# Kernel tuning notes

Measured on AMD Instinct MI355X. Metric: run time of the kernel, lower is better.

The kernel has to match this reference:

```python
import jax, jax.numpy as jnp
import numpy as np
from jax import lax

B, T, E, H = 4096, 200, 64, 64
N_USER, N_ITEM = 100000, 100000
ATT_H1, ATT_H2 = 80, 40  # DIN attention MLP sizes
FCN_IN = 4 * E + H  # user + item + hist_sum + item*hist_sum + gru2 final state


def setup_inputs() -> dict:
    key = jax.random.key(0)
    ks = jax.random.split(key, 32)
    s = 0.1
    rn = lambda k, shp: (jax.random.normal(k, shp, dtype=jnp.float32) * s)
    u = jax.random.randint(ks[0], (B,), 0, N_USER)
    i = jax.random.randint(ks[1], (B,), 0, N_ITEM)
    hist_i = jax.random.randint(ks[2], (B, T), 0, N_ITEM)
    sl = jax.random.randint(ks[3], (B,), 1, T + 1)
    mask = (jnp.arange(T)[None, :] < sl[:, None]).astype(jnp.float32)
    inp = dict(u=u, i=i, hist_i=hist_i, mask=mask)
    inp.update(
        item_emb_w=rn(ks[4], (N_ITEM, E)),
        user_emb_w=rn(ks[5], (N_USER, E)),
        # GRU1 (input dim E, hidden H): gates [r,z] fused, candidate separate (TF GRUCell layout)
        gru1_Wg=rn(ks[6], (E, 2 * H)), gru1_Ug=rn(ks[7], (H, 2 * H)), gru1_bg=jnp.zeros((2 * H,), jnp.float32),
        gru1_Wc=rn(ks[8], (E, H)), gru1_Uc=rn(ks[9], (H, H)), gru1_bc=jnp.zeros((H,), jnp.float32),
        # DIN attention MLP over [q, k, q-k, q*k]
        Wa1=rn(ks[10], (4 * H, ATT_H1)), ba1=jnp.zeros((ATT_H1,), jnp.float32),
        Wa2=rn(ks[11], (ATT_H1, ATT_H2)), ba2=jnp.zeros((ATT_H2,), jnp.float32),
        Wa3=rn(ks[12], (ATT_H2, 1)), ba3=jnp.zeros((1,), jnp.float32),
        # GRU2 (input dim H, hidden H)
        gru2_Wg=rn(ks[13], (H, 2 * H)), gru2_Ug=rn(ks[14], (H, 2 * H)), gru2_bg=jnp.zeros((2 * H,), jnp.float32),
        gru2_Wc=rn(ks[15], (H, H)), gru2_Uc=rn(ks[16], (H, H)), gru2_bc=jnp.zeros((H,), jnp.float32),
        # fcn_net: dense(2E) -> prelu -> dense(40) -> prelu -> dense(1)
        W1=rn(ks[17], (FCN_IN, 2 * E)), b1=jnp.zeros((2 * E,), jnp.float32), p1=jnp.full((2 * E,), 0.25, jnp.float32),
        W2=rn(ks[18], (2 * E, 40)), b2=jnp.zeros((40,), jnp.float32), p2=jnp.full((40,), 0.25, jnp.float32),
        W3=rn(ks[19], (40, 1)), b3=jnp.zeros((1,), jnp.float32),
    )
    return inp


def _gru(x, mask, Wg, Ug, bg, Wc, Uc, bc):
    """TF GRUCell semantics; mask freezes state past sequence length. x: [B,T,D]."""
    xg = jnp.einsum('btd,dh->bth', x, Wg) + bg  # precompute input projections
    xc = jnp.einsum('btd,dh->bth', x, Wc) + bc
    h0 = jnp.zeros((x.shape[0], Uc.shape[0]), dtype=x.dtype)

    def step(h, inp):
        xg_t, xc_t, m = inp
        r, z = jnp.split(jax.nn.sigmoid(xg_t + h @ Ug), 2, axis=-1)
        c = jnp.tanh(xc_t + (r * h) @ Uc)
        h_new = z * h + (1.0 - z) * c
        h = m[:, None] * h_new + (1.0 - m[:, None]) * h
        return h, h

    hT, hs = lax.scan(step, h0, (xg.transpose(1, 0, 2), xc.transpose(1, 0, 2), mask.T))
    return jnp.transpose(hs, (1, 0, 2)), hT  # [B,T,H], [B,H]


def _prelu(x, a):
    return jnp.where(x >= 0, x, a * x)


def reference(u, i, hist_i, mask, item_emb_w, user_emb_w,
              gru1_Wg, gru1_Ug, gru1_bg, gru1_Wc, gru1_Uc, gru1_bc,
              Wa1, ba1, Wa2, ba2, Wa3, ba3,
              gru2_Wg, gru2_Ug, gru2_bg, gru2_Wc, gru2_Uc, gru2_bc,
              W1, b1, p1, W2, b2, p2, W3, b3):
    item_eb = item_emb_w[i]            # [B,E]
    user_eb = user_emb_w[u]            # [B,E]
    hist_eb = item_emb_w[hist_i]       # [B,T,E]
    hist_sum = jnp.sum(hist_eb, axis=1)  # original uses unmasked reduce_sum

    # GRU encoder over history
    rnn1, _ = _gru(hist_eb, mask, gru1_Wg, gru1_Ug, gru1_bg, gru1_Wc, gru1_Uc, gru1_bc)

    # DIN-style attention: target item queries GRU1 states
    q = jnp.broadcast_to(item_eb[:, None, :], rnn1.shape)  # [B,T,H] (E==H)
    din = jnp.concatenate([q, rnn1, q - rnn1, q * rnn1], axis=-1)  # [B,T,4H]
    d1 = jax.nn.sigmoid(din @ Wa1 + ba1)
    d2 = jax.nn.sigmoid(d1 @ Wa2 + ba2)
    scores = (d2 @ Wa3 + ba3)[..., 0]  # [B,T]
    scores = jnp.where(mask > 0, scores, -1e9)
    alpha = jax.nn.softmax(scores, axis=-1)  # [B,T]

    # second GRU over attention-weighted states
    att_in = rnn1 * alpha[..., None]
    _, final2 = _gru(att_in, mask, gru2_Wg, gru2_Ug, gru2_bg, gru2_Wc, gru2_Uc, gru2_bc)

    # fcn_net on concatenated features
    inp = jnp.concatenate([user_eb, item_eb, hist_sum, item_eb * hist_sum, final2], axis=-1)
    h1 = _prelu(inp @ W1 + b1, p1)
    h2 = _prelu(h1 @ W2 + b2, p2)
    logits = (h2 @ W3 + b3)[:, 0]  # [B]
    return logits
```

## Files before the change

kernel.cpp:

```cpp
#include <hip/hip_runtime.h>

#define BB 4096
#define TT 200

typedef unsigned short u16;
typedef unsigned int   u32;
typedef unsigned short u16x8 __attribute__((ext_vector_type(8)));
typedef short s16x8 __attribute__((ext_vector_type(8)));
typedef float f32x4 __attribute__((ext_vector_type(4)));

__device__ __forceinline__ float bf2f(u16 u){ union{unsigned u; float f;} v; v.u=((unsigned)u)<<16; return v.f; }
__device__ __forceinline__ u16 f2bf(float f){ union{float f; unsigned u;} v; v.f=f; unsigned r=v.u + 0x7FFFu + ((v.u>>16)&1u); return (u16)(r>>16); }
__device__ __forceinline__ float sigm(float x){ return 1.0f/(1.0f+__expf(-x)); }
__device__ __forceinline__ float tanh_(float x){ return 1.0f - 2.0f/(1.0f+__expf(2.0f*x)); }

#define MFMA16(a,b,c) __builtin_amdgcn_mfma_f32_16x16x32_bf16((a),(b),(c),0,0,0)

__device__ __forceinline__ void split8(const f32x4 a, const f32x4 b, s16x8 &hi, s16x8 &lo){
#pragma unroll
  for (int j=0;j<4;j++){
    float v=a[j]; u16 h=(u16)(__float_as_uint(v)>>16);
    hi[j]=(short)h; lo[j]=(short)f2bf(v-bf2f(h));
    v=b[j]; h=(u16)(__float_as_uint(v)>>16);
    hi[j+4]=(short)h; lo[j+4]=(short)f2bf(v-bf2f(h));
  }
}


__global__ void hist_sum_kernel(const int* __restrict__ hist, const float* __restrict__ emb,
                                float* __restrict__ hs){
  int tid = blockIdx.x*256 + threadIdx.x;
  int b = tid>>3, cg = (tid&7)*8;
  float acc[8];
#pragma unroll
  for (int j=0;j<8;j++) acc[j]=0.0f;
  for (int t=0;t<TT;t++){
    int idx = hist[(size_t)b*TT+t];
    f32x4 v0=*(const f32x4*)(emb+(size_t)idx*64+cg);
    f32x4 v1=*(const f32x4*)(emb+(size_t)idx*64+cg+4);
#pragma unroll
    for (int j=0;j<4;j++){ acc[j]+=v0[j]; acc[j+4]+=v1[j]; }
  }
#pragma unroll
  for (int j=0;j<8;j++) hs[(size_t)b*64+cg+j]=acc[j];
}

__global__ __launch_bounds__(256,1) void scan1_kernel(
    const int* __restrict__ hist, const float* __restrict__ mask, const float* __restrict__ emb,
    const float* __restrict__ Wg, const float* __restrict__ Ug, const float* __restrict__ bg,
    const float* __restrict__ Wc, const float* __restrict__ Uc, const float* __restrict__ bc,
    int* __restrict__ len_g, u16* __restrict__ rnn1)
{
  __shared__ float h1buf[16][68];
  __shared__ float pbuf [16][68];
  __shared__ int   lenL [16];
  const int tid=threadIdx.x;
  const int w=tid>>6, lane=tid&63, q=lane>>4, mm=lane&15;
  const int g=blockIdx.x, b0=g*16, pb_m=b0+mm;

  if (w==0){
    int cnt=0;
    for (int t=q*50;t<q*50+50;t++) cnt += (mask[(size_t)pb_m*TT+t]!=0.0f);
    cnt += __shfl_xor(cnt,16);
    cnt += __shfl_xor(cnt,32);
    if (lane<16){ lenL[lane]=cnt; len_g[b0+lane]=cnt; }
  }
  for (int ii=tid; ii<16*68; ii+=256) (&h1buf[0][0])[ii]=0.0f;
  __syncthreads();

  int lenq[4];
#pragma unroll
  for (int r=0;r<4;r++) lenq[r]=lenL[q*4+r];
  int maxlen=1;
  for (int i=0;i<16;i++) maxlen=(lenL[i]>maxlen)?lenL[i]:maxlen;

  const int nr=16*w+mm, nz=64+16*w+mm;
  s16x8 wgr[4], wgz[4], wcf[4];
#pragma unroll
  for (int c=0;c<4;c++){
    s16x8 fr,fz,fc;
#pragma unroll
    for (int j=0;j<8;j++){
      int k=32*c+q*8+j;
      fr[j]=(short)f2bf((k<64)?Wg[(size_t)k*128+nr]:Ug[(size_t)(k-64)*128+nr]);
      fz[j]=(short)f2bf((k<64)?Wg[(size_t)k*128+nz]:Ug[(size_t)(k-64)*128+nz]);
      fc[j]=(short)f2bf((k<64)?Wc[(size_t)k*64+nr]:Uc[(size_t)(k-64)*64+nr]);
    }
    wgr[c]=fr; wgz[c]=fz; wcf[c]=fc;
  }
  const float bgr=bg[nr], bgz=bg[nz], bcv=bc[nr];

  auto load_x=[&](int t, s16x8 &a0, s16x8 &a1){
    int idx = hist[(size_t)pb_m*TT+t];
    const float* p=emb+(size_t)idx*64;
    f32x4 v0=*(const f32x4*)(p+q*8),    v1=*(const f32x4*)(p+q*8+4);
    f32x4 v2=*(const f32x4*)(p+32+q*8), v3=*(const f32x4*)(p+32+q*8+4);
    s16x8 t0,t1;
#pragma unroll
    for (int j=0;j<4;j++){
      t0[j]=(short)f2bf(v0[j]); t0[j+4]=(short)f2bf(v1[j]);
      t1[j]=(short)f2bf(v2[j]); t1[j+4]=(short)f2bf(v3[j]);
    }
    a0=t0; a1=t1;
  };

  s16x8 xf0,xf1;
  load_x(0,xf0,xf1);
  for (int t=0;t<maxlen;t++){
    s16x8 nx0,nx1;
    { int tn=(t+1<maxlen)?(t+1):(maxlen-1); load_x(tn,nx0,nx1); }

    f32x4 hA0=*(const f32x4*)&h1buf[mm][q*8];
    f32x4 hA1=*(const f32x4*)&h1buf[mm][q*8+4];
    f32x4 hB0=*(const f32x4*)&h1buf[mm][32+q*8];
    f32x4 hB1=*(const f32x4*)&h1buf[mm][32+q*8+4];
    s16x8 hhi0,hlo0,hhi1,hlo1;
    split8(hA0,hA1,hhi0,hlo0);
    split8(hB0,hB1,hhi1,hlo1);

    f32x4 ar={0.0f,0.0f,0.0f,0.0f}, az={0.0f,0.0f,0.0f,0.0f};
    ar=MFMA16(xf0 ,wgr[0],ar); az=MFMA16(xf0 ,wgz[0],az);
    ar=MFMA16(xf1 ,wgr[1],ar); az=MFMA16(xf1 ,wgz[1],az);
    ar=MFMA16(hhi0,wgr[2],ar); az=MFMA16(hhi0,wgz[2],az);
    ar=MFMA16(hhi1,wgr[3],ar); az=MFMA16(hhi1,wgz[3],az);
    ar=MFMA16(hlo0,wgr[2],ar); az=MFMA16(hlo0,wgz[2],az);
    ar=MFMA16(hlo1,wgr[3],ar); az=MFMA16(hlo1,wgz[3],az);

    float zs[4], hv[4];
#pragma unroll
    for (int r=0;r<4;r++){
      float rg=sigm(ar[r]+bgr);
      float hp=h1buf[q*4+r][16*w+mm];
      hv[r]=hp;
      pbuf[q*4+r][16*w+mm]=rg*hp;
      zs[r]=sigm(az[r]+bgz);
    }
    __syncthreads();

    f32x4 pA0=*(const f32x4*)&pbuf[mm][q*8];
    f32x4 pA1=*(const f32x4*)&pbuf[mm][q*8+4];
    f32x4 pB0=*(const f32x4*)&pbuf[mm][32+q*8];
    f32x4 pB1=*(const f32x4*)&pbuf[mm][32+q*8+4];
    s16x8 phi0,plo0,phi1,plo1;
    split8(pA0,pA1,phi0,plo0);
    split8(pB0,pB1,phi1,plo1);

    f32x4 ac={0.0f,0.0f,0.0f,0.0f};
    ac=MFMA16(xf0 ,wcf[0],ac);
    ac=MFMA16(xf1 ,wcf[1],ac);
    ac=MFMA16(phi0,wcf[2],ac);
    ac=MFMA16(phi1,wcf[3],ac);
    ac=MFMA16(plo0,wcf[2],ac);
    ac=MFMA16(plo1,wcf[3],ac);
#pragma unroll
    for (int r=0;r<4;r++){
      float c=tanh_(ac[r]+bcv);
      float z=zs[r];
      float hn=z*hv[r]+(1.0f-z)*c;
      if (t>=lenq[r]) hn=hv[r];
      h1buf[q*4+r][16*w+mm]=hn;
      rnn1[((size_t)(b0+q*4+r)*TT+t)*64 + 16*w+mm]=f2bf(hn);
    }
    __syncthreads();
    xf0=nx0; xf1=nx1;
  }
}

__global__ __launch_bounds__(64,1) void attn_kernel(
    const int* __restrict__ iidx, const float* __restrict__ emb, const u16* __restrict__ rnn1,
    const float* __restrict__ Wa1, const float* __restrict__ ba1,
    const float* __restrict__ Wa2, const float* __restrict__ ba2,
    const float* __restrict__ Wa3, const float* __restrict__ ba3,
    const int* __restrict__ len_g, float* __restrict__ scores)
{
  __shared__ u16 d1buf[16][104];
  const int lane=threadIdx.x, q=lane>>4, mm=lane&15;
  const int b=blockIdx.x;
  const int L=len_g[b];

  s16x8 w1k[5][2], wd[5][2];
#pragma unroll
  for (int nt=0;nt<5;nt++)
#pragma unroll
    for (int c=0;c<2;c++){
      s16x8 f1,f2;
#pragma unroll
      for (int j=0;j<8;j++){
        int k=32*c+q*8+j, n=16*nt+mm;
        f1[j]=(short)f2bf(Wa1[(size_t)(64+k)*80+n] - Wa1[(size_t)(128+k)*80+n]);
        f2[j]=(short)f2bf(Wa1[(size_t)(192+k)*80+n]);
      }
      w1k[nt][c]=f1; wd[nt][c]=f2;
    }
  s16x8 w2f[3][3];
#pragma unroll
  for (int nt=0;nt<3;nt++)
#pragma unroll
    for (int c=0;c<3;c++){
      s16x8 f;
#pragma unroll
      for (int j=0;j<8;j++){
        int k=32*c+q*8+j, n=16*nt+mm;
        f[j]=(short)((k<80 && n<40)?f2bf(Wa2[(size_t)k*40+n]):0);
      }
      w2f[nt][c]=f;
    }
  float ba2v[3], w3v[3];
#pragma unroll
  for (int nt=0;nt<3;nt++){ int n=16*nt+mm; ba2v[nt]=(n<40)?ba2[n]:0.0f; w3v[nt]=(n<40)?Wa3[n]:0.0f; }
  const float ba3v=ba3[0];

  const int ib=iidx[b];
  float qv0[8], qv1[8];
  s16x8 aq0,aq1;
#pragma unroll
  for (int j=0;j<8;j++){
    qv0[j]=emb[(size_t)ib*64+q*8+j];
    qv1[j]=emb[(size_t)ib*64+32+q*8+j];
    aq0[j]=(short)f2bf(qv0[j]); aq1[j]=(short)f2bf(qv1[j]);
  }
  float pre[5];
#pragma unroll
  for (int nt=0;nt<5;nt++){
    int n=16*nt+mm;
    s16x8 bp0,bp1;
#pragma unroll
    for (int j=0;j<8;j++){
      int k=q*8+j, k2=32+q*8+j;
      bp0[j]=(short)f2bf(Wa1[(size_t)k *80+n]+Wa1[(size_t)(128+k )*80+n]);
      bp1[j]=(short)f2bf(Wa1[(size_t)k2*80+n]+Wa1[(size_t)(128+k2)*80+n]);
    }
    f32x4 a={0.0f,0.0f,0.0f,0.0f};
    a=MFMA16(aq0,bp0,a); a=MFMA16(aq1,bp1,a);
    pre[nt]=a[0]+ba1[n];
  }

  for (int ii=lane; ii<16*104; ii+=64) (&d1buf[0][0])[ii]=0;
  __syncthreads();

  const int nch=(L+15)>>4;
  for (int ch=0; ch<nch; ch++){
    int t0=ch*16;
    size_t base=((size_t)b*TT + t0+mm)*64;
    s16x8 kf0=*(const s16x8*)(rnn1+base+q*8);
    s16x8 kf1=*(const s16x8*)(rnn1+base+32+q*8);
    s16x8 kq0,kq1;
#pragma unroll
    for (int j=0;j<8;j++){
      kq0[j]=(short)f2bf(bf2f((u16)kf0[j])*qv0[j]);
      kq1[j]=(short)f2bf(bf2f((u16)kf1[j])*qv1[j]);
    }
    f32x4 acc[5];
#pragma unroll
    for (int nt=0;nt<5;nt++){
      f32x4 a={pre[nt],pre[nt],pre[nt],pre[nt]};
      a=MFMA16(kf0,w1k[nt][0],a); a=MFMA16(kf1,w1k[nt][1],a);
      a=MFMA16(kq0,wd[nt][0],a);  a=MFMA16(kq1,wd[nt][1],a);
      acc[nt]=a;
    }
#pragma unroll
    for (int nt=0;nt<5;nt++)
#pragma unroll
      for (int r=0;r<4;r++)
        d1buf[q*4+r][16*nt+mm]=f2bf(sigm(acc[nt][r]));
    __syncthreads();
    s16x8 a0=*(const s16x8*)&d1buf[mm][q*8];
    s16x8 a1=*(const s16x8*)&d1buf[mm][32+q*8];
    s16x8 a2=*(const s16x8*)&d1buf[mm][64+q*8];
    f32x4 acc2[3];
#pragma unroll
    for (int nt=0;nt<3;nt++){
      f32x4 a={0.0f,0.0f,0.0f,0.0f};
      a=MFMA16(a0,w2f[nt][0],a); a=MFMA16(a1,w2f[nt][1],a); a=MFMA16(a2,w2f[nt][2],a);
      acc2[nt]=a;
    }
    float part[4];
#pragma unroll
    for (int r=0;r<4;r++){
      float s=0.0f;
#pragma unroll
      for (int nt=0;nt<3;nt++) s+=sigm(acc2[nt][r]+ba2v[nt])*w3v[nt];
      part[r]=s;
    }
#pragma unroll
    for (int d=1;d<16;d<<=1)
#pragma unroll
      for (int r=0;r<4;r++) part[r]+=__shfl_xor(part[r],d);
    if (mm==0){
#pragma unroll
      for (int r=0;r<4;r++){ int t=t0+q*4+r; if (t<TT) scores[(size_t)b*TT+t]=part[r]+ba3v; }
    }
    __syncthreads();
  }
}

__global__ __launch_bounds__(64,1) void softmax_kernel(const int* __restrict__ len_g, float* __restrict__ sc){
  const int b=blockIdx.x, lane=threadIdx.x;
  const int L=len_g[b];
  float mx=-3e38f;
  for (int t=lane;t<L;t+=64) mx=fmaxf(mx,sc[(size_t)b*TT+t]);
#pragma unroll
  for (int d=1;d<64;d<<=1) mx=fmaxf(mx,__shfl_xor(mx,d));
  float sm=0.0f;
  for (int t=lane;t<L;t+=64) sm+=__expf(sc[(size_t)b*TT+t]-mx);
#pragma unroll
  for (int d=1;d<64;d<<=1) sm+=__shfl_xor(sm,d);
  float inv=1.0f/sm;
  for (int t=lane;t<TT;t+=64){
    float v=(t<L)?__expf(sc[(size_t)b*TT+t]-mx)*inv:0.0f;
    sc[(size_t)b*TT+t]=v;
  }
}

__global__ __launch_bounds__(256,1) void scan2_kernel(
    const u16* __restrict__ rnn1, const float* __restrict__ alpha, const int* __restrict__ len_g,
    const float* __restrict__ Wg, const float* __restrict__ Ug, const float* __restrict__ bg,
    const float* __restrict__ Wc, const float* __restrict__ Uc, const float* __restrict__ bc,
    float* __restrict__ f2)
{
  __shared__ float h2buf[16][68];
  __shared__ float pbuf [16][68];
  __shared__ int   lenL [16];
  const int tid=threadIdx.x;
  const int w=tid>>6, lane=tid&63, q=lane>>4, mm=lane&15;
  const int g=blockIdx.x, b0=g*16, pb_m=b0+mm;

  if (tid<16) lenL[tid]=len_g[b0+tid];
  for (int ii=tid; ii<16*68; ii+=256) (&h2buf[0][0])[ii]=0.0f;
  __syncthreads();

  int lenq[4];
#pragma unroll
  for (int r=0;r<4;r++) lenq[r]=lenL[q*4+r];
  int maxlen=1;
  for (int i=0;i<16;i++) maxlen=(lenL[i]>maxlen)?lenL[i]:maxlen;

  const int nr=16*w+mm, nz=64+16*w+mm;
  s16x8 wgr[4], wgz[4], wcf[4];
#pragma unroll
  for (int c=0;c<4;c++){
    s16x8 fr,fz,fc;
#pragma unroll
    for (int j=0;j<8;j++){
      int k=32*c+q*8+j;
      fr[j]=(short)f2bf((k<64)?Wg[(size_t)k*128+nr]:Ug[(size_t)(k-64)*128+nr]);
      fz[j]=(short)f2bf((k<64)?Wg[(size_t)k*128+nz]:Ug[(size_t)(k-64)*128+nz]);
      fc[j]=(short)f2bf((k<64)?Wc[(size_t)k*64+nr]:Uc[(size_t)(k-64)*64+nr]);
    }
    wgr[c]=fr; wgz[c]=fz; wcf[c]=fc;
  }
  const float bgr=bg[nr], bgz=bg[nz], bcv=bc[nr];

  auto load_x=[&](int t, s16x8 &a0, s16x8 &a1){
    size_t base=((size_t)pb_m*TT+t)*64;
    u16x8 k0=*(const u16x8*)(rnn1+base+q*8);
    u16x8 k1=*(const u16x8*)(rnn1+base+32+q*8);
    float al=alpha[(size_t)pb_m*TT+t];
    s16x8 t0,t1;
#pragma unroll
    for (int j=0;j<8;j++){
      t0[j]=(short)f2bf(bf2f(k0[j])*al);
      t1[j]=(short)f2bf(bf2f(k1[j])*al);
    }
    a0=t0; a1=t1;
  };

  s16x8 xf0,xf1;
  load_x(0,xf0,xf1);
  for (int t=0;t<maxlen;t++){
    s16x8 nx0,nx1;
    { int tn=(t+1<maxlen)?(t+1):(maxlen-1); load_x(tn,nx0,nx1); }

    f32x4 hA0=*(const f32x4*)&h2buf[mm][q*8];
    f32x4 hA1=*(const f32x4*)&h2buf[mm][q*8+4];
    f32x4 hB0=*(const f32x4*)&h2buf[mm][32+q*8];
    f32x4 hB1=*(const f32x4*)&h2buf[mm][32+q*8+4];
    s16x8 hhi0,hlo0,hhi1,hlo1;
    split8(hA0,hA1,hhi0,hlo0);
    split8(hB0,hB1,hhi1,hlo1);

    f32x4 ar={0.0f,0.0f,0.0f,0.0f}, az={0.0f,0.0f,0.0f,0.0f};
    ar=MFMA16(xf0 ,wgr[0],ar); az=MFMA16(xf0 ,wgz[0],az);
    ar=MFMA16(xf1 ,wgr[1],ar); az=MFMA16(xf1 ,wgz[1],az);
    ar=MFMA16(hhi0,wgr[2],ar); az=MFMA16(hhi0,wgz[2],az);
    ar=MFMA16(hhi1,wgr[3],ar); az=MFMA16(hhi1,wgz[3],az);
    ar=MFMA16(hlo0,wgr[2],ar); az=MFMA16(hlo0,wgz[2],az);
    ar=MFMA16(hlo1,wgr[3],ar); az=MFMA16(hlo1,wgz[3],az);

    float zs[4], hv[4];
#pragma unroll
    for (int r=0;r<4;r++){
      float rg=sigm(ar[r]+bgr);
      float hp=h2buf[q*4+r][16*w+mm];
      hv[r]=hp;
      pbuf[q*4+r][16*w+mm]=rg*hp;
      zs[r]=sigm(az[r]+bgz);
    }
    __syncthreads();

    f32x4 pA0=*(const f32x4*)&pbuf[mm][q*8];
    f32x4 pA1=*(const f32x4*)&pbuf[mm][q*8+4];
    f32x4 pB0=*(const f32x4*)&pbuf[mm][32+q*8];
    f32x4 pB1=*(const f32x4*)&pbuf[mm][32+q*8+4];
    s16x8 phi0,plo0,phi1,plo1;
    split8(pA0,pA1,phi0,plo0);
    split8(pB0,pB1,phi1,plo1);

    f32x4 ac={0.0f,0.0f,0.0f,0.0f};
    ac=MFMA16(xf0 ,wcf[0],ac);
    ac=MFMA16(xf1 ,wcf[1],ac);
    ac=MFMA16(phi0,wcf[2],ac);
    ac=MFMA16(phi1,wcf[3],ac);
    ac=MFMA16(plo0,wcf[2],ac);
    ac=MFMA16(plo1,wcf[3],ac);
#pragma unroll
    for (int r=0;r<4;r++){
      float c=tanh_(ac[r]+bcv);
      float z=zs[r];
      float hn=z*hv[r]+(1.0f-z)*c;
      if (t>=lenq[r]) hn=hv[r];
      h2buf[q*4+r][16*w+mm]=hn;
    }
    __syncthreads();
    xf0=nx0; xf1=nx1;
  }

#pragma unroll
  for (int r=0;r<4;r++)
    f2[(size_t)(b0+q*4+r)*64 + 16*w+mm]=h2buf[q*4+r][16*w+mm];
}

__global__ __launch_bounds__(64,1) void fcn_kernel(
    const int* __restrict__ uidx, const int* __restrict__ iidx,
    const float* __restrict__ uemb, const float* __restrict__ emb,
    const float* __restrict__ hs, const float* __restrict__ f2,
    const float* __restrict__ Wf1, const float* __restrict__ fb1, const float* __restrict__ fp1,
    const float* __restrict__ Wf2, const float* __restrict__ fb2, const float* __restrict__ fp2,
    const float* __restrict__ Wf3, const float* __restrict__ fb3,
    float* __restrict__ out)
{
  __shared__ float inL[16][320];
  __shared__ u16   h1L[16][128];
  __shared__ float h2o[16][40];
  const int lane=threadIdx.x, q=lane>>4, mm=lane&15;
  const int b0=blockIdx.x*16;

  {
    int row=lane>>2, sub=lane&3;
    int b=b0+row;
    int ub=uidx[b], ibv=iidx[b];
    for (int c=sub*80;c<sub*80+80;c++){
      int seg=c>>6, f=c&63; float v;
      if      (seg==0) v=uemb[(size_t)ub*64+f];
      else if (seg==1) v=emb[(size_t)ibv*64+f];
      else if (seg==2) v=hs[(size_t)b*64+f];
      else if (seg==3) v=emb[(size_t)ibv*64+f]*hs[(size_t)b*64+f];
      else             v=f2[(size_t)b*64+f];
      inL[row][c]=v;
    }
  }
  __syncthreads();

  {
    f32x4 acc1[8];
#pragma unroll
    for (int nt=0;nt<8;nt++) acc1[nt]=f32x4{0.0f,0.0f,0.0f,0.0f};
#pragma unroll
    for (int kc=0;kc<10;kc++){
      s16x8 af;
#pragma unroll
      for (int j=0;j<8;j++) af[j]=(short)f2bf(inL[mm][32*kc+q*8+j]);
#pragma unroll
      for (int nt=0;nt<8;nt++){
        s16x8 bfr;
#pragma unroll
        for (int j=0;j<8;j++) bfr[j]=(short)f2bf(Wf1[(size_t)(32*kc+q*8+j)*128 + 16*nt+mm]);
        acc1[nt]=MFMA16(af,bfr,acc1[nt]);
      }
    }
#pragma unroll
    for (int nt=0;nt<8;nt++)
#pragma unroll
      for (int r=0;r<4;r++){
        int col=16*nt+mm, row=q*4+r;
        float x=acc1[nt][r]+fb1[col];
        float pp=fp1[col];
        h1L[row][col]=f2bf((x>=0.0f)?x:pp*x);
      }
  }
  __syncthreads();

  {
    f32x4 acc2[3];
#pragma unroll
    for (int nt=0;nt<3;nt++) acc2[nt]=f32x4{0.0f,0.0f,0.0f,0.0f};
#pragma unroll
    for (int kc=0;kc<4;kc++){
      s16x8 af=*(const s16x8*)&h1L[mm][32*kc+q*8];
#pragma unroll
      for (int nt=0;nt<3;nt++){
        s16x8 bfr;
#pragma unroll
        for (int j=0;j<8;j++){
          int k=32*kc+q*8+j, n=16*nt+mm;
          bfr[j]=(short)((n<40)?f2bf(Wf2[(size_t)k*40+n]):0);
        }
        acc2[nt]=MFMA16(af,bfr,acc2[nt]);
      }
    }
#pragma unroll
    for (int nt=0;nt<3;nt++)
#pragma unroll
      for (int r=0;r<4;r++){
        int col=16*nt+mm, row=q*4+r;
        if (col<40){
          float x=acc2[nt][r]+fb2[col];
          float pp=fp2[col];
          h2o[row][col]=(x>=0.0f)?x:pp*x;
        }
      }
  }
  __syncthreads();

  {
    int row=lane>>2, sub=lane&3;
    float s=0.0f;
    for (int k=sub;k<40;k+=4) s+=h2o[row][k]*Wf3[k];
    s+=__shfl_xor(s,1); s+=__shfl_xor(s,2);
    if (sub==0) out[b0+row]=s+fb3[0];
  }
}

template<bool F32>
__global__ __launch_bounds__(64,1) void dien_mega_kernel(
    const int* __restrict__ uidx, const int* __restrict__ iidx,
    const int* __restrict__ hist, const void* __restrict__ mask,
    const void* __restrict__ emb,  const void* __restrict__ uemb,
    const void* __restrict__ W1g, const void* __restrict__ U1g, const void* __restrict__ g1bg,
    const void* __restrict__ W1c, const void* __restrict__ U1c, const void* __restrict__ g1bc,
    const void* __restrict__ Wa1, const void* __restrict__ ba1,
    const void* __restrict__ Wa2, const void* __restrict__ ba2,
    const void* __restrict__ Wa3, const void* __restrict__ ba3,
    const void* __restrict__ W2g, const void* __restrict__ U2g, const void* __restrict__ g2bg,
    const void* __restrict__ W2c, const void* __restrict__ U2c, const void* __restrict__ g2bc,
    const void* __restrict__ Wf1, const void* __restrict__ fb1, const void* __restrict__ fp1,
    const void* __restrict__ Wf2, const void* __restrict__ fb2, const void* __restrict__ fp2,
    const void* __restrict__ Wf3, const void* __restrict__ fb3,
    void* __restrict__ outp)
{
  auto LF=[&](const void* p, size_t i)->float {
    return F32 ? ((const float*)p)[i] : bf2f(((const u16*)p)[i]);
  };
  auto LB=[&](const void* p, size_t i)->u16 {
    return F32 ? f2bf(((const float*)p)[i]) : ((const u16*)p)[i];
  };
  auto FR8=[&](const void* p, size_t off)->s16x8 {
    s16x8 f;
    if (F32){
      const float* pp=(const float*)p+off;
      f32x4 a=*(const f32x4*)pp, b=*(const f32x4*)(pp+4);
#pragma unroll
      for (int j=0;j<4;j++){ f[j]=(short)f2bf(a[j]); f[j+4]=(short)f2bf(b[j]); }
    } else {
      f=*(const s16x8*)((const u16*)p+off);
    }
    return f;
  };

  __shared__ float h1buf[16][68];
  __shared__ float h2buf[16][68];
  __shared__ float pbuf [16][68];
  __shared__ u16   d1buf[16][104];
  __shared__ u16   scL  [16][200];
  __shared__ float hsL  [16][64];
  __shared__ s16x8 u2gL [16][64];
  __shared__ s16x8 u2cL [ 8][64];
  __shared__ float h2o  [16][40];
  __shared__ u16   ueL  [16][64];
  __shared__ u16   ieL  [16][64];
  __shared__ int   lenL [16];

  const int lane=threadIdx.x, q=lane>>4, mm=lane&15;
  const int g=blockIdx.x, b0=g*16;
  const int pb_m=b0+mm;

  {
    int cnt=0;
    for (int t=q*50;t<q*50+50;t++) cnt += (LF(mask,(size_t)pb_m*TT+t)!=0.0f);
    cnt += __shfl_xor(cnt,16);
    cnt += __shfl_xor(cnt,32);
    if (lane<16) lenL[lane]=cnt;
  }
  __syncthreads();
  int lenq[4];
#pragma unroll
// ... 401 lines not shown
        a=MFMA16(hlo0,wh0,a);
        a=MFMA16(hlo1,wh1,a);
        ga[nt]=a;
      }
      float zs[4][4], hv[4][4];
#pragma unroll
      for (int nt=0;nt<4;nt++)
#pragma unroll
        for (int r=0;r<4;r++){
          float rg=sigm(ga[nt][r]+b2gv[nt]);
          float h_=h2buf[q*4+r][16*nt+mm];
          hv[nt][r]=h_;
          pbuf[q*4+r][16*nt+mm]=rg*h_;
          zs[nt][r]=sigm(ga[nt+4][r]+b2gv[nt+4]);
        }
      __syncthreads();
      f32x4 pA0=*(const f32x4*)&pbuf[mm][q*8];
      f32x4 pA1=*(const f32x4*)&pbuf[mm][q*8+4];
      f32x4 pB0=*(const f32x4*)&pbuf[mm][32+q*8];
      f32x4 pB1=*(const f32x4*)&pbuf[mm][32+q*8+4];
      s16x8 phi0,plo0,phi1,plo1;
      split8(pA0,pA1,phi0,plo0);
      split8(pB0,pB1,phi1,plo1);
      f32x4 ca[4];
#pragma unroll
      for (int nt=0;nt<4;nt++){
        s16x8 wh0=u2cL[nt*2+0][lane];
        s16x8 wh1=u2cL[nt*2+1][lane];
        f32x4 a={0.0f,0.0f,0.0f,0.0f};
        a=MFMA16(af0 ,wc2x[nt][0],a);
        a=MFMA16(af1 ,wc2x[nt][1],a);
        a=MFMA16(phi0,wh0,a);
        a=MFMA16(phi1,wh1,a);
        a=MFMA16(plo0,wh0,a);
        a=MFMA16(plo1,wh1,a);
        ca[nt]=a;
      }
#pragma unroll
      for (int nt=0;nt<4;nt++)
#pragma unroll
        for (int r=0;r<4;r++){
          float c=tanh_(ca[nt][r]+b2cv[nt]);
          float z=zs[nt][r];
          float hn=z*hv[nt][r]+(1.0f-z)*c;
          if (t>=lenq[r]) hn=hv[nt][r];
          h2buf[q*4+r][16*nt+mm]=hn;
        }
      __syncthreads();
    }

    xf0=nx0; xf1=nx1;
  }

  {
    int row=lane>>2, c0=(lane&3)*16;
    int ub=uidx[b0+row], ibv=iidx[b0+row];
#pragma unroll
    for (int j=0;j<16;j++){
      ueL[row][c0+j]=LB(uemb,(size_t)ub*64+c0+j);
      ieL[row][c0+j]=LB(emb ,(size_t)ibv*64+c0+j);
    }
  }
  __syncthreads();

  {
    f32x4 acc1[8];
#pragma unroll
    for (int nt=0;nt<8;nt++) acc1[nt]=f32x4{0.0f,0.0f,0.0f,0.0f};
#pragma unroll
    for (int kc=0;kc<10;kc++){
      const int seg=kc>>1, off=(kc&1)*32+q*8;
      s16x8 af;
#pragma unroll
      for (int j=0;j<8;j++){
        int f=off+j;
        u16 v;
        if      (seg==0) v=ueL[mm][f];
        else if (seg==1) v=ieL[mm][f];
        else if (seg==2) v=f2bf(hsL[mm][f]);
        else if (seg==3) v=f2bf(bf2f(ieL[mm][f])*hsL[mm][f]);
        else             v=f2bf(h2buf[mm][f]);
        af[j]=(short)v;
      }
#pragma unroll
      for (int nt=0;nt<8;nt++){
        s16x8 bfr;
#pragma unroll
        for (int j=0;j<8;j++) bfr[j]=(short)LB(Wf1,(size_t)(32*kc+q*8+j)*128 + 16*nt+mm);
        acc1[nt]=MFMA16(af,bfr,acc1[nt]);
      }
    }
    __syncthreads();
#pragma unroll
    for (int nt=0;nt<8;nt++)
#pragma unroll
      for (int r=0;r<4;r++){
        int col=16*nt+mm, row=q*4+r;
        float x=acc1[nt][r]+LF(fb1,col);
        float pp=LF(fp1,col);
        scL[row][col]=f2bf((x>=0.0f)?x:pp*x);
      }
  }
  __syncthreads();

  {
    f32x4 acc2[3];
#pragma unroll
    for (int nt=0;nt<3;nt++) acc2[nt]=f32x4{0.0f,0.0f,0.0f,0.0f};
#pragma unroll
    for (int kc=0;kc<4;kc++){
      s16x8 af=*(const s16x8*)&scL[mm][32*kc+q*8];
#pragma unroll
      for (int nt=0;nt<3;nt++){
        s16x8 bfr;
#pragma unroll
        for (int j=0;j<8;j++){
          int k=32*kc+q*8+j, n=16*nt+mm;
          bfr[j]=(short)((n<40)?LB(Wf2,(size_t)k*40+n):0);
        }
        acc2[nt]=MFMA16(af,bfr,acc2[nt]);
      }
    }
#pragma unroll
    for (int nt=0;nt<3;nt++)
#pragma unroll
      for (int r=0;r<4;r++){
        int col=16*nt+mm, row=q*4+r;
        if (col<40){
          float x=acc2[nt][r]+LF(fb2,col);
          float pp=LF(fp2,col);
          h2o[row][col]=(x>=0.0f)?x:pp*x;
        }
      }
  }
  __syncthreads();

  {
    int row=lane>>2, sub=lane&3;
    float s=0.0f;
    for (int k=sub;k<40;k+=4) s+=h2o[row][k]*LF(Wf3,k);
    s+=__shfl_xor(s,1); s+=__shfl_xor(s,2);
    if (sub==0){
      float v=s+LF(fb3,0);
      if (F32) ((float*)outp)[b0+row]=v;
      else     ((u16*) outp)[b0+row]=f2bf(v);
    }
  }
}

extern "C" void kernel_launch(void* const* d_in, const int* in_sizes, int n_in,
                              void* d_out, int out_size, void* d_ws, size_t ws_size,
                              hipStream_t stream)
{
  (void)in_sizes; (void)n_in; (void)out_size;
  const int* u    =(const int*)d_in[0];
  const int* it   =(const int*)d_in[1];
  const int* hist =(const int*)d_in[2];
  const float* mask=(const float*)d_in[3];
  const float* item_emb=(const float*)d_in[4];
  const float* user_emb=(const float*)d_in[5];
  const float* g1Wg=(const float*)d_in[6],  *g1Ug=(const float*)d_in[7],  *g1bg=(const float*)d_in[8];
  const float* g1Wc=(const float*)d_in[9],  *g1Uc=(const float*)d_in[10], *g1bc=(const float*)d_in[11];
  const float* Wa1=(const float*)d_in[12], *ba1=(const float*)d_in[13];
  const float* Wa2=(const float*)d_in[14], *ba2=(const float*)d_in[15];
  const float* Wa3=(const float*)d_in[16], *ba3=(const float*)d_in[17];
  const float* g2Wg=(const float*)d_in[18], *g2Ug=(const float*)d_in[19], *g2bg=(const float*)d_in[20];
  const float* g2Wc=(const float*)d_in[21], *g2Uc=(const float*)d_in[22], *g2bc=(const float*)d_in[23];
  const float* W1=(const float*)d_in[24], *b1=(const float*)d_in[25], *p1=(const float*)d_in[26];
  const float* W2=(const float*)d_in[27], *b2=(const float*)d_in[28], *p2=(const float*)d_in[29];
  const float* W3=(const float*)d_in[30], *b3=(const float*)d_in[31];

  const size_t sz_rnn1  =(size_t)BB*TT*64*2;
  const size_t sz_scores=(size_t)BB*TT*4;
  const size_t sz_len   =(size_t)BB*4;
  const size_t sz_hs    =(size_t)BB*64*4;
  const size_t sz_f2    =(size_t)BB*64*4;
  const size_t NEED = sz_rnn1+sz_scores+sz_len+sz_hs+sz_f2 + 1024;

  if (ws_size >= NEED){
    char* ws=(char*)d_ws;
    u16*   rnn1  =(u16*)  ws;                    ws+=sz_rnn1;
    float* scores=(float*)ws;                    ws+=sz_scores;
    int*   len_g =(int*)  ws;                    ws+=sz_len;
    float* hs    =(float*)ws;                    ws+=sz_hs;
    float* f2    =(float*)ws;

    hist_sum_kernel<<<BB*8/256,256,0,stream>>>(hist, item_emb, hs);
    scan1_kernel   <<<BB/16,   256,0,stream>>>(hist, mask, item_emb,
                                               g1Wg,g1Ug,g1bg,g1Wc,g1Uc,g1bc,
                                               len_g, rnn1);
    attn_kernel    <<<BB,       64,0,stream>>>(it, item_emb, rnn1,
                                               Wa1,ba1,Wa2,ba2,Wa3,ba3,
                                               len_g, scores);
    softmax_kernel <<<BB,       64,0,stream>>>(len_g, scores);
    scan2_kernel   <<<BB/16,   256,0,stream>>>(rnn1, scores, len_g,
                                               g2Wg,g2Ug,g2bg,g2Wc,g2Uc,g2bc,
                                               f2);
    fcn_kernel     <<<BB/16,    64,0,stream>>>(u, it, user_emb, item_emb, hs, f2,
                                               W1,b1,p1,W2,b2,p2,W3,b3,
                                               (float*)d_out);
  } else {
    dien_mega_kernel<true><<<BB/16, 64, 0, stream>>>(
        u, it, hist, mask, item_emb, user_emb,
        g1Wg,g1Ug,g1bg,g1Wc,g1Uc,g1bc,
        Wa1,ba1,Wa2,ba2,Wa3,ba3,
        g2Wg,g2Ug,g2bg,g2Wc,g2Uc,g2bc,
        W1,b1,p1,W2,b2,p2,W3,b3,
        d_out);
  }
}
```

Measured before the change: 909.9 us.

## Fuse softmax into attention, pre-convert embeddings to bf16, keep GRU state split in LDS

Adds a pass that converts the item embedding table to bf16 once per call, and both hist_sum and scan1 now gather half-width rows from that copy. Softmax and the alpha scaling move into the attention kernel, which writes a bf16 attention-weighted input for scan2, so the separate softmax launch and the per-step scaling inside scan2 go away. The GRU scans keep the hidden state in registers and store pre-split bf16 hi/lo halves in LDS instead of fp32, so the splitting is no longer repeated per reader. Each MFMA chain is split into two accumulators to shorten dependency chains. The costs are converting the whole 100k-row table on every call, an extra write and read of a full B×T×64 bf16 tensor, and bf16 rounding applied to hist_sum inputs.

```diff
diff --git a/kernel.cpp b/kernel.cpp
--- a/kernel.cpp
+++ b/kernel.cpp
@@ -27,7 +27,17 @@
 }
 
 
-__global__ void hist_sum_kernel(const int* __restrict__ hist, const float* __restrict__ emb,
+__global__ void conv_kernel(const float* __restrict__ src, u16* __restrict__ dst, int n){
+  int i=(blockIdx.x*256+threadIdx.x)*8;
+  if (i>=n) return;
+  f32x4 a=*(const f32x4*)(src+i), b=*(const f32x4*)(src+i+4);
+  u16x8 o;
+#pragma unroll
+  for (int j=0;j<4;j++){ o[j]=f2bf(a[j]); o[j+4]=f2bf(b[j]); }
+  *(u16x8*)(dst+i)=o;
+}
+
+__global__ void hist_sum_kernel(const int* __restrict__ hist, const u16* __restrict__ emb16,
                                 float* __restrict__ hs){
   int tid = blockIdx.x*256 + threadIdx.x;
   int b = tid>>3, cg = (tid&7)*8;
@@ -36,24 +46,25 @@
   for (int j=0;j<8;j++) acc[j]=0.0f;
   for (int t=0;t<TT;t++){
     int idx = hist[(size_t)b*TT+t];
-    f32x4 v0=*(const f32x4*)(emb+(size_t)idx*64+cg);
-    f32x4 v1=*(const f32x4*)(emb+(size_t)idx*64+cg+4);
-#pragma unroll
-    for (int j=0;j<4;j++){ acc[j]+=v0[j]; acc[j+4]+=v1[j]; }
+    u16x8 v=*(const u16x8*)(emb16+(size_t)idx*64+cg);
+#pragma unroll
+    for (int j=0;j<8;j++) acc[j]+=bf2f(v[j]);
   }
 #pragma unroll
   for (int j=0;j<8;j++) hs[(size_t)b*64+cg+j]=acc[j];
 }
 
 __global__ __launch_bounds__(256,1) void scan1_kernel(
-    const int* __restrict__ hist, const float* __restrict__ mask, const float* __restrict__ emb,
+    const int* __restrict__ hist, const float* __restrict__ mask, const u16* __restrict__ emb16,
     const float* __restrict__ Wg, const float* __restrict__ Ug, const float* __restrict__ bg,
     const float* __restrict__ Wc, const float* __restrict__ Uc, const float* __restrict__ bc,
     int* __restrict__ len_g, u16* __restrict__ rnn1)
 {
-  __shared__ float h1buf[16][68];
-  __shared__ float pbuf [16][68];
-  __shared__ int   lenL [16];
+  __shared__ __attribute__((aligned(16))) u16 hhiL[16][72];
+  __shared__ __attribute__((aligned(16))) u16 hloL[16][72];
+  __shared__ __attribute__((aligned(16))) u16 phiL[16][72];
+  __shared__ __attribute__((aligned(16))) u16 ploL[16][72];
+  __shared__ int lenL[16];
   const int tid=threadIdx.x;
   const int w=tid>>6, lane=tid&63, q=lane>>4, mm=lane&15;
   const int g=blockIdx.x, b0=g*16, pb_m=b0+mm;
@@ -65,7 +76,7 @@
     cnt += __shfl_xor(cnt,32);
     if (lane<16){ lenL[lane]=cnt; len_g[b0+lane]=cnt; }
   }
-  for (int ii=tid; ii<16*68; ii+=256) (&h1buf[0][0])[ii]=0.0f;
+  for (int ii=tid; ii<16*72; ii+=256){ (&hhiL[0][0])[ii]=0; (&hloL[0][0])[ii]=0; }
   __syncthreads();
 
   int lenq[4];
@@ -90,18 +101,13 @@
   }
   const float bgr=bg[nr], bgz=bg[nz], bcv=bc[nr];
 
+  float hreg[4]={0.0f,0.0f,0.0f,0.0f};
+
   auto load_x=[&](int t, s16x8 &a0, s16x8 &a1){
     int idx = hist[(size_t)pb_m*TT+t];
-    const float* p=emb+(size_t)idx*64;
-    f32x4 v0=*(const f32x4*)(p+q*8),    v1=*(const f32x4*)(p+q*8+4);
-    f32x4 v2=*(const f32x4*)(p+32+q*8), v3=*(const f32x4*)(p+32+q*8+4);
-    s16x8 t0,t1;
-#pragma unroll
-    for (int j=0;j<4;j++){
-      t0[j]=(short)f2bf(v0[j]); t0[j+4]=(short)f2bf(v1[j]);
-      t1[j]=(short)f2bf(v2[j]); t1[j+4]=(short)f2bf(v3[j]);
-    }
-    a0=t0; a1=t1;
+    const u16* p=emb16+(size_t)idx*64;
+    a0=*(const s16x8*)(p+q*8);
+    a1=*(const s16x8*)(p+32+q*8);
   };
 
   s16x8 xf0,xf1;
@@ -110,56 +116,56 @@
     s16x8 nx0,nx1;
     { int tn=(t+1<maxlen)?(t+1):(maxlen-1); load_x(tn,nx0,nx1); }
 
-    f32x4 hA0=*(const f32x4*)&h1buf[mm][q*8];
-    f32x4 hA1=*(const f32x4*)&h1buf[mm][q*8+4];
-    f32x4 hB0=*(const f32x4*)&h1buf[mm][32+q*8];
-    f32x4 hB1=*(const f32x4*)&h1buf[mm][32+q*8+4];
-    s16x8 hhi0,hlo0,hhi1,hlo1;
-    split8(hA0,hA1,hhi0,hlo0);
-    split8(hB0,hB1,hhi1,hlo1);
-
-    f32x4 ar={0.0f,0.0f,0.0f,0.0f}, az={0.0f,0.0f,0.0f,0.0f};
-    ar=MFMA16(xf0 ,wgr[0],ar); az=MFMA16(xf0 ,wgz[0],az);
-    ar=MFMA16(xf1 ,wgr[1],ar); az=MFMA16(xf1 ,wgz[1],az);
-    ar=MFMA16(hhi0,wgr[2],ar); az=MFMA16(hhi0,wgz[2],az);
-    ar=MFMA16(hhi1,wgr[3],ar); az=MFMA16(hhi1,wgz[3],az);
-    ar=MFMA16(hlo0,wgr[2],ar); az=MFMA16(hlo0,wgz[2],az);
-    ar=MFMA16(hlo1,wgr[3],ar); az=MFMA16(hlo1,wgz[3],az);
-
-    float zs[4], hv[4];
+    s16x8 hhi0=*(const s16x8*)&hhiL[mm][q*8];
+    s16x8 hhi1=*(const s16x8*)&hhiL[mm][32+q*8];
+    s16x8 hlo0=*(const s16x8*)&hloL[mm][q*8];
+    s16x8 hlo1=*(const s16x8*)&hloL[mm][32+q*8];
+
+    f32x4 ar0={0.0f,0.0f,0.0f,0.0f}, ar1={0.0f,0.0f,0.0f,0.0f};
+    f32x4 az0={0.0f,0.0f,0.0f,0.0f}, az1={0.0f,0.0f,0.0f,0.0f};
+    ar0=MFMA16(xf0 ,wgr[0],ar0); az0=MFMA16(xf0 ,wgz[0],az0);
+    ar0=MFMA16(xf1 ,wgr[1],ar0); az0=MFMA16(xf1 ,wgz[1],az0);
+    ar0=MFMA16(hhi0,wgr[2],ar0); az0=MFMA16(hhi0,wgz[2],az0);
+    ar1=MFMA16(hhi1,wgr[3],ar1); az1=MFMA16(hhi1,wgz[3],az1);
+    ar1=MFMA16(hlo0,wgr[2],ar1); az1=MFMA16(hlo0,wgz[2],az1);
+    ar1=MFMA16(hlo1,wgr[3],ar1); az1=MFMA16(hlo1,wgz[3],az1);
+    f32x4 ar=ar0+ar1, az=az0+az1;
+
+    float zs[4];
 #pragma unroll
     for (int r=0;r<4;r++){
       float rg=sigm(ar[r]+bgr);
-      float hp=h1buf[q*4+r][16*w+mm];
-      hv[r]=hp;
-      pbuf[q*4+r][16*w+mm]=rg*hp;
+      float pv=rg*hreg[r];
+      u16 ph=(u16)(__float_as_uint(pv)>>16);
+      phiL[q*4+r][16*w+mm]=ph;
+      ploL[q*4+r][16*w+mm]=f2bf(pv-bf2f(ph));
       zs[r]=sigm(az[r]+bgz);
     }
     __syncthreads();
 
-    f32x4 pA0=*(const f32x4*)&pbuf[mm][q*8];
-    f32x4 pA1=*(const f32x4*)&pbuf[mm][q*8+4];
-    f32x4 pB0=*(const f32x4*)&pbuf[mm][32+q*8];
-    f32x4 pB1=*(const f32x4*)&pbuf[mm][32+q*8+4];
-    s16x8 phi0,plo0,phi1,plo1;
-    split8(pA0,pA1,phi0,plo0);
-    split8(pB0,pB1,phi1,plo1);
-
-    f32x4 ac={0.0f,0.0f,0.0f,0.0f};
-    ac=MFMA16(xf0 ,wcf[0],ac);
-    ac=MFMA16(xf1 ,wcf[1],ac);
-    ac=MFMA16(phi0,wcf[2],ac);
-    ac=MFMA16(phi1,wcf[3],ac);
-    ac=MFMA16(plo0,wcf[2],ac);
-    ac=MFMA16(plo1,wcf[3],ac);
+    s16x8 phi0=*(const s16x8*)&phiL[mm][q*8];
+    s16x8 phi1=*(const s16x8*)&phiL[mm][32+q*8];
+    s16x8 plo0=*(const s16x8*)&ploL[mm][q*8];
+    s16x8 plo1=*(const s16x8*)&ploL[mm][32+q*8];
+
+    f32x4 ac0={0.0f,0.0f,0.0f,0.0f}, ac1={0.0f,0.0f,0.0f,0.0f};
+    ac0=MFMA16(xf0 ,wcf[0],ac0);
+    ac0=MFMA16(xf1 ,wcf[1],ac0);
+    ac0=MFMA16(phi0,wcf[2],ac0);
+    ac1=MFMA16(phi1,wcf[3],ac1);
+    ac1=MFMA16(plo0,wcf[2],ac1);
+    ac1=MFMA16(plo1,wcf[3],ac1);
+    f32x4 ac=ac0+ac1;
 #pragma unroll
     for (int r=0;r<4;r++){
       float c=tanh_(ac[r]+bcv);
-      float z=zs[r];
-      float hn=z*hv[r]+(1.0f-z)*c;
-      if (t>=lenq[r]) hn=hv[r];
-      h1buf[q*4+r][16*w+mm]=hn;
-      rnn1[((size_t)(b0+q*4+r)*TT+t)*64 + 16*w+mm]=f2bf(hn);
+      float hn=zs[r]*hreg[r]+(1.0f-zs[r])*c;
+      if (t>=lenq[r]) hn=hreg[r];
+      hreg[r]=hn;
+      u16 hh=f2bf(hn);
+      hhiL[q*4+r][16*w+mm]=hh;
+      hloL[q*4+r][16*w+mm]=f2bf(hn-bf2f(hh));
+      rnn1[((size_t)(b0+q*4+r)*TT+t)*64 + 16*w+mm]=hh;
     }
     __syncthreads();
     xf0=nx0; xf1=nx1;
@@ -171,9 +177,10 @@
     const float* __restrict__ Wa1, const float* __restrict__ ba1,
     const float* __restrict__ Wa2, const float* __restrict__ ba2,
     const float* __restrict__ Wa3, const float* __restrict__ ba3,
-    const int* __restrict__ len_g, float* __restrict__ scores)
+    const int* __restrict__ len_g, u16* __restrict__ attin)
 {
-  __shared__ u16 d1buf[16][104];
+  __shared__ __attribute__((aligned(16))) u16 d1buf[16][104];
+  __shared__ float scS[208];
   const int lane=threadIdx.x, q=lane>>4, mm=lane&15;
   const int b=blockIdx.x;
   const int L=len_g[b];
@@ -236,6 +243,7 @@
   }
 
   for (int ii=lane; ii<16*104; ii+=64) (&d1buf[0][0])[ii]=0;
+  for (int t=lane;t<208;t+=64) scS[t]=-1e9f;
   __syncthreads();
 
   const int nch=(L+15)>>4;
@@ -288,45 +296,53 @@
       for (int r=0;r<4;r++) part[r]+=__shfl_xor(part[r],d);
     if (mm==0){
 #pragma unroll
-      for (int r=0;r<4;r++){ int t=t0+q*4+r; if (t<TT) scores[(size_t)b*TT+t]=part[r]+ba3v; }
+      for (int r=0;r<4;r++){ int t=t0+q*4+r; scS[t]=(t<L)?(part[r]+ba3v):-1e9f; }
     }
     __syncthreads();
   }
-}
-
-__global__ __launch_bounds__(64,1) void softmax_kernel(const int* __restrict__ len_g, float* __restrict__ sc){
-  const int b=blockIdx.x, lane=threadIdx.x;
-  const int L=len_g[b];
+
   float mx=-3e38f;
-  for (int t=lane;t<L;t+=64) mx=fmaxf(mx,sc[(size_t)b*TT+t]);
+  for (int t=lane;t<TT;t+=64) mx=fmaxf(mx,scS[t]);
 #pragma unroll
   for (int d=1;d<64;d<<=1) mx=fmaxf(mx,__shfl_xor(mx,d));
   float sm=0.0f;
-  for (int t=lane;t<L;t+=64) sm+=__expf(sc[(size_t)b*TT+t]-mx);
+  for (int t=lane;t<TT;t+=64) sm+=__expf(scS[t]-mx);
 #pragma unroll
   for (int d=1;d<64;d<<=1) sm+=__shfl_xor(sm,d);
   float inv=1.0f/sm;
-  for (int t=lane;t<TT;t+=64){
-    float v=(t<L)?__expf(sc[(size_t)b*TT+t]-mx)*inv:0.0f;
-    sc[(size_t)b*TT+t]=v;
+
+  {
+    int toff=lane>>3, cg=(lane&7)*8;
+    for (int t0=0;t0<TT;t0+=8){
+      int tt=t0+toff;
+      float al=(tt<L)?(__expf(scS[tt]-mx)*inv):0.0f;
+      size_t base=((size_t)b*TT+tt)*64+cg;
+      u16x8 kk=*(const u16x8*)(rnn1+base);
+      s16x8 o;
+#pragma unroll
+      for (int j=0;j<8;j++) o[j]=(short)f2bf(bf2f(kk[j])*al);
+      *(s16x8*)(attin+base)=o;
+    }
   }
 }
 
 __global__ __launch_bounds__(256,1) void scan2_kernel(
-    const u16* __restrict__ rnn1, const float* __restrict__ alpha, const int* __restrict__ len_g,
+    const u16* __restrict__ attin, const int* __restrict__ len_g,
     const float* __restrict__ Wg, const float* __restrict__ Ug, const float* __restrict__ bg,
     const float* __restrict__ Wc, const float* __restrict__ Uc, const float* __restrict__ bc,
     float* __restrict__ f2)
 {
-  __shared__ float h2buf[16][68];
-  __shared__ float pbuf [16][68];
-  __shared__ int   lenL [16];
+  __shared__ __attribute__((aligned(16))) u16 hhiL[16][72];
+  __shared__ __attribute__((aligned(16))) u16 hloL[16][72];
+  __shared__ __attribute__((aligned(16))) u16 phiL[16][72];
+  __shared__ __attribute__((aligned(16))) u16 ploL[16][72];
+  __shared__ int lenL[16];
   const int tid=threadIdx.x;
   const int w=tid>>6, lane=tid&63, q=lane>>4, mm=lane&15;
   const int g=blockIdx.x, b0=g*16, pb_m=b0+mm;
 
   if (tid<16) lenL[tid]=len_g[b0+tid];
-  for (int ii=tid; ii<16*68; ii+=256) (&h2buf[0][0])[ii]=0.0f;
+  for (int ii=tid; ii<16*72; ii+=256){ (&hhiL[0][0])[ii]=0; (&hloL[0][0])[ii]=0; }
   __syncthreads();
 
   int lenq[4];
@@ -351,18 +367,12 @@
   }
   const float bgr=bg[nr], bgz=bg[nz], bcv=bc[nr];
 
+  float hreg[4]={0.0f,0.0f,0.0f,0.0f};
+
   auto load_x=[&](int t, s16x8 &a0, s16x8 &a1){
     size_t base=((size_t)pb_m*TT+t)*64;
-    u16x8 k0=*(const u16x8*)(rnn1+base+q*8);
-    u16x8 k1=*(const u16x8*)(rnn1+base+32+q*8);
-    float al=alpha[(size_t)pb_m*TT+t];
-    s16x8 t0,t1;
-#pragma unroll
-    for (int j=0;j<8;j++){
-      t0[j]=(short)f2bf(bf2f(k0[j])*al);
-      t1[j]=(short)f2bf(bf2f(k1[j])*al);
-    }
-    a0=t0; a1=t1;
+    a0=*(const s16x8*)(attin+base+q*8);
+    a1=*(const s16x8*)(attin+base+32+q*8);
   };
 
   s16x8 xf0,xf1;
@@ -371,55 +381,55 @@
     s16x8 nx0,nx1;
     { int tn=(t+1<maxlen)?(t+1):(maxlen-1); load_x(tn,nx0,nx1); }
 
-    f32x4 hA0=*(const f32x4*)&h2buf[mm][q*8];
-    f32x4 hA1=*(const f32x4*)&h2buf[mm][q*8+4];
-    f32x4 hB0=*(const f32x4*)&h2buf[mm][32+q*8];
-    f32x4 hB1=*(const f32x4*)&h2buf[mm][32+q*8+4];
-    s16x8 hhi0,hlo0,hhi1,hlo1;
-    split8(hA0,hA1,hhi0,hlo0);
-    split8(hB0,hB1,hhi1,hlo1);
-
-    f32x4 ar={0.0f,0.0f,0.0f,0.0f}, az={0.0f,0.0f,0.0f,0.0f};
-    ar=MFMA16(xf0 ,wgr[0],ar); az=MFMA16(xf0 ,wgz[0],az);
-    ar=MFMA16(xf1 ,wgr[1],ar); az=MFMA16(xf1 ,wgz[1],az);
-    ar=MFMA16(hhi0,wgr[2],ar); az=MFMA16(hhi0,wgz[2],az);
-    ar=MFMA16(hhi1,wgr[3],ar); az=MFMA16(hhi1,wgz[3],az);
-    ar=MFMA16(hlo0,wgr[2],ar); az=MFMA16(hlo0,wgz[2],az);
-    ar=MFMA16(hlo1,wgr[3],ar); az=MFMA16(hlo1,wgz[3],az);
-
-    float zs[4], hv[4];
+    s16x8 hhi0=*(const s16x8*)&hhiL[mm][q*8];
+    s16x8 hhi1=*(const s16x8*)&hhiL[mm][32+q*8];
+    s16x8 hlo0=*(const s16x8*)&hloL[mm][q*8];
+    s16x8 hlo1=*(const s16x8*)&hloL[mm][32+q*8];
+
+    f32x4 ar0={0.0f,0.0f,0.0f,0.0f}, ar1={0.0f,0.0f,0.0f,0.0f};
+    f32x4 az0={0.0f,0.0f,0.0f,0.0f}, az1={0.0f,0.0f,0.0f,0.0f};
+    ar0=MFMA16(xf0 ,wgr[0],ar0); az0=MFMA16(xf0 ,wgz[0],az0);
+    ar0=MFMA16(xf1 ,wgr[1],ar0); az0=MFMA16(xf1 ,wgz[1],az0);
+    ar0=MFMA16(hhi0,wgr[2],ar0); az0=MFMA16(hhi0,wgz[2],az0);
+    ar1=MFMA16(hhi1,wgr[3],ar1); az1=MFMA16(hhi1,wgz[3],az1);
+    ar1=MFMA16(hlo0,wgr[2],ar1); az1=MFMA16(hlo0,wgz[2],az1);
+    ar1=MFMA16(hlo1,wgr[3],ar1); az1=MFMA16(hlo1,wgz[3],az1);
+    f32x4 ar=ar0+ar1, az=az0+az1;
+
+    float zs[4];
 #pragma unroll
     for (int r=0;r<4;r++){
       float rg=sigm(ar[r]+bgr);
-      float hp=h2buf[q*4+r][16*w+mm];
-      hv[r]=hp;
-      pbuf[q*4+r][16*w+mm]=rg*hp;
+      float pv=rg*hreg[r];
+      u16 ph=(u16)(__float_as_uint(pv)>>16);
+      phiL[q*4+r][16*w+mm]=ph;
+      ploL[q*4+r][16*w+mm]=f2bf(pv-bf2f(ph));
       zs[r]=sigm(az[r]+bgz);
     }
     __syncthreads();
 
-    f32x4 pA0=*(const f32x4*)&pbuf[mm][q*8];
-    f32x4 pA1=*(const f32x4*)&pbuf[mm][q*8+4];
-    f32x4 pB0=*(const f32x4*)&pbuf[mm][32+q*8];
-    f32x4 pB1=*(const f32x4*)&pbuf[mm][32+q*8+4];
-    s16x8 phi0,plo0,phi1,plo1;
-    split8(pA0,pA1,phi0,plo0);
-    split8(pB0,pB1,phi1,plo1);
-
-    f32x4 ac={0.0f,0.0f,0.0f,0.0f};
-    ac=MFMA16(xf0 ,wcf[0],ac);
-    ac=MFMA16(xf1 ,wcf[1],ac);
-    ac=MFMA16(phi0,wcf[2],ac);
-    ac=MFMA16(phi1,wcf[3],ac);
-    ac=MFMA16(plo0,wcf[2],ac);
-    ac=MFMA16(plo1,wcf[3],ac);
+    s16x8 phi0=*(const s16x8*)&phiL[mm][q*8];
+    s16x8 phi1=*(const s16x8*)&phiL[mm][32+q*8];
+    s16x8 plo0=*(const s16x8*)&ploL[mm][q*8];
+    s16x8 plo1=*(const s16x8*)&ploL[mm][32+q*8];
+
+    f32x4 ac0={0.0f,0.0f,0.0f,0.0f}, ac1={0.0f,0.0f,0.0f,0.0f};
+    ac0=MFMA16(xf0 ,wcf[0],ac0);
+    ac0=MFMA16(xf1 ,wcf[1],ac0);
+    ac0=MFMA16(phi0,wcf[2],ac0);
+    ac1=MFMA16(phi1,wcf[3],ac1);
+    ac1=MFMA16(plo0,wcf[2],ac1);
+    ac1=MFMA16(plo1,wcf[3],ac1);
+    f32x4 ac=ac0+ac1;
 #pragma unroll
     for (int r=0;r<4;r++){
       float c=tanh_(ac[r]+bcv);
-      float z=zs[r];
-      float hn=z*hv[r]+(1.0f-z)*c;
-      if (t>=lenq[r]) hn=hv[r];
-      h2buf[q*4+r][16*w+mm]=hn;
+      float hn=zs[r]*hreg[r]+(1.0f-zs[r])*c;
+      if (t>=lenq[r]) hn=hreg[r];
+      hreg[r]=hn;
+      u16 hh=f2bf(hn);
+      hhiL[q*4+r][16*w+mm]=hh;
+      hloL[q*4+r][16*w+mm]=f2bf(hn-bf2f(hh));
     }
     __syncthreads();
     xf0=nx0; xf1=nx1;
@@ -427,7 +437,7 @@
 
 #pragma unroll
   for (int r=0;r<4;r++)
-    f2[(size_t)(b0+q*4+r)*64 + 16*w+mm]=h2buf[q*4+r][16*w+mm];
+    f2[(size_t)(b0+q*4+r)*64 + 16*w+mm]=hreg[r];
 }
 
 __global__ __launch_bounds__(64,1) void fcn_kernel(
@@ -440,7 +450,7 @@
     float* __restrict__ out)
 {
   __shared__ float inL[16][320];
-  __shared__ u16   h1L[16][128];
+  __shared__ __attribute__((aligned(16))) u16 h1L[16][128];
   __shared__ float h2o[16][40];
   const int lane=threadIdx.x, q=lane>>4, mm=lane&15;
   const int b0=blockIdx.x*16;
@@ -1148,7 +1158,7 @@
                               void* d_out, int out_size, void* d_ws, size_t ws_size,
                               hipStream_t stream)
 {
-  (void)in_sizes; (void)n_in; (void)out_size;
+  (void)n_in; (void)out_size;
   const int* u    =(const int*)d_in[0];
   const int* it   =(const int*)d_in[1];
   const int* hist =(const int*)d_in[2];
@@ -1166,33 +1176,36 @@
   const float* W2=(const float*)d_in[27], *b2=(const float*)d_in[28], *p2=(const float*)d_in[29];
   const float* W3=(const float*)d_in[30], *b3=(const float*)d_in[31];
 
-  const size_t sz_rnn1  =(size_t)BB*TT*64*2;
-  const size_t sz_scores=(size_t)BB*TT*4;
-  const size_t sz_len   =(size_t)BB*4;
-  const size_t sz_hs    =(size_t)BB*64*4;
-  const size_t sz_f2    =(size_t)BB*64*4;
-  const size_t NEED = sz_rnn1+sz_scores+sz_len+sz_hs+sz_f2 + 1024;
+  const int emb_n = in_sizes[4];
+  const size_t sz_rnn1 =(size_t)BB*TT*64*2;
+  const size_t sz_attin=(size_t)BB*TT*64*2;
+  const size_t sz_emb16=(((size_t)emb_n*2)+255)&~(size_t)255;
+  const size_t sz_len  =(((size_t)BB*4)+255)&~(size_t)255;
+  const size_t sz_hs   =(size_t)BB*64*4;
+  const size_t sz_f2   =(size_t)BB*64*4;
+  const size_t NEED = sz_rnn1+sz_attin+sz_emb16+sz_len+sz_hs+sz_f2 + 1024;
 
   if (ws_size >= NEED){
     char* ws=(char*)d_ws;
-    u16*   rnn1  =(u16*)  ws;                    ws+=sz_rnn1;
-    float* scores=(float*)ws;                    ws+=sz_scores;
-    int*   len_g =(int*)  ws;                    ws+=sz_len;
-    float* hs    =(float*)ws;                    ws+=sz_hs;
-    float* f2    =(float*)ws;
-
-    hist_sum_kernel<<<BB*8/256,256,0,stream>>>(hist, item_emb, hs);
-    scan1_kernel   <<<BB/16,   256,0,stream>>>(hist, mask, item_emb,
+    u16*   rnn1 =(u16*)ws;   ws+=sz_rnn1;
+    u16*   attin=(u16*)ws;   ws+=sz_attin;
+    u16*   emb16=(u16*)ws;   ws+=sz_emb16;
+    int*   len_g=(int*)ws;   ws+=sz_len;
+    float* hs   =(float*)ws; ws+=sz_hs;
+    float* f2   =(float*)ws;
+
+    conv_kernel    <<<(emb_n/8+255)/256,256,0,stream>>>(item_emb, emb16, emb_n);
+    hist_sum_kernel<<<BB*8/256,256,0,stream>>>(hist, emb16, hs);
+    scan1_kernel   <<<BB/16, 256, 0, stream>>>(hist, mask, emb16,
                                                g1Wg,g1Ug,g1bg,g1Wc,g1Uc,g1bc,
                                                len_g, rnn1);
-    attn_kernel    <<<BB,       64,0,stream>>>(it, item_emb, rnn1,
+    attn_kernel    <<<BB,     64, 0, stream>>>(it, item_emb, rnn1,
                                                Wa1,ba1,Wa2,ba2,Wa3,ba3,
-                                               len_g, scores);
-    softmax_kernel <<<BB,       64,0,stream>>>(len_g, scores);
-    scan2_kernel   <<<BB/16,   256,0,stream>>>(rnn1, scores, len_g,
+                                               len_g, attin);
+    scan2_kernel   <<<BB/16, 256, 0, stream>>>(attin, len_g,
                                                g2Wg,g2Ug,g2bg,g2Wc,g2Uc,g2bc,
                                                f2);
-    fcn_kernel     <<<BB/16,    64,0,stream>>>(u, it, user_emb, item_emb, hs, f2,
+    fcn_kernel     <<<BB/16,  64, 0, stream>>>(u, it, user_emb, item_emb, hs, f2,
                                                W1,b1,p1,W2,b2,p2,W3,b3,
                                                (float*)d_out);
   } else {
```

New measurement: 895.6 us. Within noise of the previous version (-1.6%).
